# Optimization experiments

Hardware: AMD Instinct MI355X
Metric: run time of the kernel (lower is better)

The kernel has to match this reference:

```python
import jax, jax.numpy as jnp
import numpy as np

E, H = 1024, 16
HD = E // H
QLEN, KLEN, BS = 1024, 2048, 4
PREV = KLEN - QLEN


def _rel_shift(x):
    # x: (q, k, b, h) -> Transformer-XL relative shift
    q, k, b, h = x.shape
    x = jnp.pad(x, ((0, 0), (1, 0), (0, 0), (0, 0)))  # (q, k+1, b, h)
    x = x.reshape(k + 1, q, b, h)[1:].reshape(q, k, b, h)
    return x


def setup_inputs() -> dict:
    key = jax.random.key(0)
    ks = jax.random.split(key, 16)
    s = 0.02  # weight init scale
    inp = {
        "query": jax.random.normal(ks[0], (QLEN, BS, E), jnp.float32),
        "key": jax.random.normal(ks[1], (KLEN, BS, E), jnp.float32),
        "value": jax.random.normal(ks[2], (KLEN, BS, E), jnp.float32),
        "pos_embedding": jax.random.normal(ks[3], (KLEN, 1, E), jnp.float32),
        "U": jax.random.normal(ks[4], (H, HD), jnp.float32) * s,
        "V": jax.random.normal(ks[5], (H, HD), jnp.float32) * s,
        "Wq": jax.random.normal(ks[6], (E, E), jnp.float32) * s,
        "bq": jnp.zeros((E,), jnp.float32),
        "Wk": jax.random.normal(ks[7], (E, E), jnp.float32) * s,
        "bk": jnp.zeros((E,), jnp.float32),
        "Wv": jax.random.normal(ks[8], (E, E), jnp.float32) * s,
        "bv": jnp.zeros((E,), jnp.float32),
        "Wp": jax.random.normal(ks[9], (E, E), jnp.float32) * s,
        "Wo": jax.random.normal(ks[10], (E, E), jnp.float32) * s,
        "bo": jnp.zeros((E,), jnp.float32),
    }
    # causal XL mask: query i attends to keys j <= i + PREV; True = masked
    qi = jnp.arange(QLEN)[:, None]
    kj = jnp.arange(KLEN)[None, :]
    inp["mask"] = (kj > qi + PREV)[:, :, None]  # (q, k, 1) bool
    return inp


def reference(query, key, value, pos_embedding, U, V, Wq, bq, Wk, bk, Wv, bv, Wp, Wo, bo, mask):
    q_len, b, e = query.shape
    k_len = key.shape[0]
    scale = float(np.sqrt(e))  # note: sqrt(embed_dim), as in the source

    queries = (query @ Wq + bq).reshape(q_len, b, H, HD)
    keys = (key @ Wk + bk).reshape(k_len, b, H, HD)
    values = (value @ Wv + bv).reshape(k_len, b, H, HD)
    R = (pos_embedding @ Wp).reshape(-1, H, HD)  # (k, H, HD)

    content_score = jnp.einsum('qbhd,kbhd->qkbh', queries + U, keys)
    position_score = jnp.einsum('qbhd,khd->qkbh', queries + V, R)
    position_score = _rel_shift(position_score)

    attention_score = (content_score + position_score) / scale
    attention_score = jnp.where(mask[..., None], jnp.float32(-1e20), attention_score)
    attention = jax.nn.softmax(attention_score, axis=1)

    alpha = jnp.einsum('qkbh,kbhd->qbhd', attention, values).reshape(q_len, b, e)
    return alpha @ Wo + bo
```

## Files before the change

### kernel.cpp

```cpp
#include <hip/hip_runtime.h>
#include <stdint.h>

#define QLEN 1024
#define KLEN 2048
#define BSZ  4
#define NH   16
#define HD   64
#define EMB  1024
#define PREVL 1024
#define SLOG2E 0.045084220027780106f

typedef __attribute__((ext_vector_type(4))) float f32x4;
typedef __attribute__((ext_vector_type(8))) short bf16x8;
typedef __attribute__((ext_vector_type(4))) short bf16x4;

__device__ __forceinline__ unsigned short f2bf(float f){
  unsigned u = __float_as_uint(f);
  u += 0x7fffu + ((u >> 16) & 1u);
  return (unsigned short)(u >> 16);
}

__device__ __forceinline__ void gload_lds16(const void* g, void* l){
  __builtin_amdgcn_global_load_lds((const __attribute__((address_space(1))) void*)g,
                                   (__attribute__((address_space(3))) void*)l, 16, 0, 0);
}

__global__ void txl_transpose5(const float* __restrict__ w0, const float* __restrict__ w1,
                               const float* __restrict__ w2, const float* __restrict__ w3,
                               const float* __restrict__ w4,
                               unsigned short* __restrict__ o0, unsigned short* __restrict__ o1,
                               unsigned short* __restrict__ o2, unsigned short* __restrict__ o3,
                               unsigned short* __restrict__ o4){
  const float* in; unsigned short* out;
  switch (blockIdx.z){
    case 0: in = w0; out = o0; break;
    case 1: in = w1; out = o1; break;
    case 2: in = w2; out = o2; break;
    case 3: in = w3; out = o3; break;
    default: in = w4; out = o4; break;
  }
  __shared__ float tile[32][33];
  int tx = threadIdx.x, ty = threadIdx.y;
  int k0 = blockIdx.y * 32, n0 = blockIdx.x * 32;
  #pragma unroll
  for (int j = 0; j < 32; j += 8)
    tile[ty + j][tx] = in[(size_t)(k0 + ty + j) * EMB + n0 + tx];
  __syncthreads();
  #pragma unroll
  for (int j = 0; j < 32; j += 8)
    out[(size_t)(n0 + ty + j) * EMB + k0 + tx] = f2bf(tile[tx][ty + j]);
}

__global__ void txl_cvt(const float* __restrict__ q, const float* __restrict__ k,
                        const float* __restrict__ v, const float* __restrict__ p,
                        unsigned short* __restrict__ qo, unsigned short* __restrict__ ko,
                        unsigned short* __restrict__ vo, unsigned short* __restrict__ po){
  for (size_t c = (size_t)blockIdx.x * 256 + threadIdx.x; c < 2883584; c += (size_t)2048 * 256){
    const float* src; unsigned short* dst; size_t off;
    if (c < 524288)      { src = q; dst = qo; off = c; }
    else if (c < 1572864){ src = k; dst = ko; off = c - 524288; }
    else if (c < 2621440){ src = v; dst = vo; off = c - 1572864; }
    else                 { src = p; dst = po; off = c - 2621440; }
    f32x4 a = *(const f32x4*)(src + off * 8);
    f32x4 b = *(const f32x4*)(src + off * 8 + 4);
    bf16x8 r;
    #pragma unroll
    for (int u = 0; u < 4; ++u){ r[u] = (short)f2bf(a[u]); r[u + 4] = (short)f2bf(b[u]); }
    *(bf16x8*)(dst + off * 8) = r;
  }
}

template<int MODE>
__global__ __launch_bounds__(256)
void txl_gemm(const unsigned short* __restrict__ Ag, const unsigned short* __restrict__ Wt,
              const float* __restrict__ bias, const float* __restrict__ Ub,
              const float* __restrict__ Vb, void* __restrict__ out0,
              void* __restrict__ out1){
  const int tid = threadIdx.x;
  const int lane = tid & 63, wave = tid >> 6;
  const int lr = lane & 15, lg = lane >> 4;
  const int wm = wave >> 1, wn = wave & 1;
  const int m0 = blockIdx.y * 128, n0 = blockIdx.x * 128;
  __shared__ unsigned short At[128 * 64];
  __shared__ unsigned short Bt[128 * 64];
  f32x4 acc[4][4] = {};

  for (int kt = 0; kt < EMB / 64; ++kt){
    const int k0 = kt * 64;
    __syncthreads();
    #pragma unroll
    for (int j = 0; j < 4; ++j){
      int row = j * 32 + (tid >> 3);
      int g = (tid & 7) ^ (row & 7);
      gload_lds16(Ag + (size_t)(m0 + row) * EMB + k0 + g * 8, &At[j * 2048 + wave * 512]);
      gload_lds16(Wt + (size_t)(n0 + row) * EMB + k0 + g * 8, &Bt[j * 2048 + wave * 512]);
    }
    __syncthreads();
    #pragma unroll
    for (int ks = 0; ks < 2; ++ks){
      bf16x8 af[4], bfr[4];
      #pragma unroll
      for (int mb = 0; mb < 4; ++mb){
        int row = wm * 64 + mb * 16 + lr;
        af[mb] = *(const bf16x8*)&At[row * 64 + ((lg + 4 * ks) ^ (row & 7)) * 8];
      }
      #pragma unroll
      for (int nb = 0; nb < 4; ++nb){
        int row = wn * 64 + nb * 16 + lr;
        bfr[nb] = *(const bf16x8*)&Bt[row * 64 + ((lg + 4 * ks) ^ (row & 7)) * 8];
      }
      __builtin_amdgcn_s_setprio(1);
      #pragma unroll
      for (int mb = 0; mb < 4; ++mb)
        #pragma unroll
        for (int nb = 0; nb < 4; ++nb)
          acc[mb][nb] = __builtin_amdgcn_mfma_f32_16x16x32_bf16(af[mb], bfr[nb], acc[mb][nb], 0, 0, 0);
      __builtin_amdgcn_s_setprio(0);
    }
  }
  #pragma unroll
  for (int mb = 0; mb < 4; ++mb){
    #pragma unroll
    for (int nb = 0; nb < 4; ++nb){
      #pragma unroll
      for (int i = 0; i < 4; ++i){
        int m = m0 + wm * 64 + mb * 16 + 4 * lg + i;
        int n = n0 + wn * 64 + nb * 16 + lr;
        float v = acc[mb][nb][i];
        if constexpr (MODE == 0){
          int q = m >> 2, b = m & 3, h = n >> 6, d = n & 63;
          size_t idx = ((((size_t)b * NH + h) * QLEN) + q) * HD + d;
          float base = v + bias[n];
          ((unsigned short*)out0)[idx] = f2bf((base + Ub[n]) * SLOG2E);
          ((unsigned short*)out1)[idx] = f2bf((base + Vb[n]) * SLOG2E);
        } else if constexpr (MODE == 1){
          int kp = m >> 2, b = m & 3, h = n >> 6, d = n & 63;
          ((unsigned short*)out0)[((((size_t)b * NH + h) * KLEN) + kp) * HD + d] = f2bf(v + bias[n]);
        } else if constexpr (MODE == 2){
          int kp = m >> 2, b = m & 3, h = n >> 6, d = n & 63;
          ((unsigned short*)out0)[((((size_t)b * NH + h) * HD) + d) * KLEN + kp] = f2bf(v + bias[n]);
        } else if constexpr (MODE == 3){
          int h = n >> 6, d = n & 63;
          ((unsigned short*)out0)[((size_t)h * KLEN + m) * HD + d] = f2bf(v);
        } else {
          ((float*)out0)[(size_t)m * EMB + n] = v + bias[n];
        }
      }
    }
  }
}

__global__ __launch_bounds__(256)
void txl_attn(const unsigned short* __restrict__ Qu, const unsigned short* __restrict__ Qv,
              const unsigned short* __restrict__ Kb, const unsigned short* __restrict__ Vt,
              const unsigned short* __restrict__ Rb, unsigned short* __restrict__ alpha){
  const int tid = threadIdx.x, lane = tid & 63, wave = tid >> 6;
  const int lr = lane & 15, lg = lane >> 4;
  const int qt = blockIdx.x, h = blockIdx.y, b = blockIdx.z;
  const int q0 = qt * 64;
  const int myq0 = q0 + 16 * wave;

  __shared__ union { unsigned short q[2][64 * 64]; unsigned short p[4][16 * 64]; } smq;
  __shared__ unsigned short sm_k[64 * 64];
  __shared__ unsigned short sm_v[64 * 64];
  __shared__ unsigned short sm_r[128 * 64];
  __shared__ float sm_t[4][16 * 81];

  const unsigned short* quB = Qu + (((size_t)b * NH + h) * QLEN) * HD;
  const unsigned short* qvB = Qv + (((size_t)b * NH + h) * QLEN) * HD;
  const unsigned short* kB  = Kb + (((size_t)b * NH + h) * KLEN) * HD;
  const unsigned short* vB  = Vt + (((size_t)b * NH + h) * HD) * KLEN;
  const unsigned short* rB  = Rb + ((size_t)h * KLEN) * HD;

  #pragma unroll
  for (int j = 0; j < 2; ++j){
    int row = j * 32 + (tid >> 3);
    int g = (tid & 7) ^ (row & 7);
    gload_lds16(quB + (size_t)(q0 + row) * HD + g * 8, &smq.q[0][j * 2048 + wave * 512]);
    gload_lds16(qvB + (size_t)(q0 + row) * HD + g * 8, &smq.q[1][j * 2048 + wave * 512]);
  }
  __syncthreads();
  bf16x8 qfu[2], qfv[2];
  {
    int row = 16 * wave + lr;
    #pragma unroll
    for (int ks = 0; ks < 2; ++ks){
      qfu[ks] = *(const bf16x8*)&smq.q[0][row * 64 + ((lg + 4 * ks) ^ (row & 7)) * 8];
      qfv[ks] = *(const bf16x8*)&smq.q[1][row * 64 + ((lg + 4 * ks) ^ (row & 7)) * 8];
    }
  }

  f32x4 o[4] = {};
  float ls[4] = {0.f, 0.f, 0.f, 0.f};

  const int nk0 = qt + 17;
  const int nk = nk0 < 32 ? nk0 : 32;
  const int roff = 48 - 16 * wave;

  for (int kt = 0; kt < nk; ++kt){
    const int k0 = kt * 64;
    const int rbase = k0 + (QLEN - 64) - q0;
    __syncthreads();
    #pragma unroll
    for (int j = 0; j < 2; ++j){
      int row = j * 32 + (tid >> 3);
      int g = (tid & 7) ^ (row & 7);
      gload_lds16(kB + (size_t)(k0 + row) * HD + g * 8, &sm_k[j * 2048 + wave * 512]);
      gload_lds16(vB + (size_t)row * KLEN + k0 + g * 8, &sm_v[j * 2048 + wave * 512]);
    }
    #pragma unroll
    for (int j = 0; j < 4; ++j){
      int row = j * 32 + (tid >> 3);
      int g = (tid & 7) ^ (row & 7);
      int r = rbase + row; if (r > KLEN - 1) r = KLEN - 1;
      gload_lds16(rB + (size_t)r * HD + g * 8, &sm_r[j * 2048 + wave * 512]);
    }
    __syncthreads();

    f32x4 sc[4] = {};
    f32x4 tt[5] = {};
    __builtin_amdgcn_s_setprio(1);
    #pragma unroll
    for (int ks = 0; ks < 2; ++ks){
      #pragma unroll
      for (int nb = 0; nb < 4; ++nb){
        int row = nb * 16 + lr;
        bf16x8 kf = *(const bf16x8*)&sm_k[row * 64 + ((lg + 4 * ks) ^ (row & 7)) * 8];
        sc[nb] = __builtin_amdgcn_mfma_f32_16x16x32_bf16(qfu[ks], kf, sc[nb], 0, 0, 0);
      }
      #pragma unroll
      for (int rb = 0; rb < 5; ++rb){
        int row = roff + rb * 16 + lr;
        bf16x8 rf = *(const bf16x8*)&sm_r[row * 64 + ((lg + 4 * ks) ^ (row & 7)) * 8];
        tt[rb] = __builtin_amdgcn_mfma_f32_16x16x32_bf16(qfv[ks], rf, tt[rb], 0, 0, 0);
      }
    }
    __builtin_amdgcn_s_setprio(0);

    float* tw = sm_t[wave];
    #pragma unroll
    for (int rb = 0; rb < 5; ++rb)
      #pragma unroll
      for (int i = 0; i < 4; ++i)
        tw[(4 * lg + i) * 81 + rb * 16 + lr] = tt[rb][i];
    asm volatile("s_waitcnt lgkmcnt(0)" ::: "memory");

    #pragma unroll
    for (int i = 0; i < 4; ++i){
      int qq = 4 * lg + i;
      int qglob = myq0 + qq;
      float rs = 0.f;
      #pragma unroll
      for (int nb = 0; nb < 4; ++nb){
        int kk = nb * 16 + lr;
        float tv = tw[qq * 81 + kk + 15 - qq];
        float s = sc[nb][i] + tv;
        if (k0 + kk > qglob + PREVL) s = -1e30f;
        float p = exp2f(s);
        rs += p;
        smq.p[wave][qq * 64 + (((kk >> 3) ^ (qq & 7)) << 3) + (kk & 7)] = f2bf(p);
      }
      ls[i] += rs;
    }
    asm volatile("s_waitcnt lgkmcnt(0)" ::: "memory");

    __builtin_amdgcn_s_setprio(1);
    #pragma unroll
    for (int ks = 0; ks < 2; ++ks){
      bf16x8 pa = *(const bf16x8*)&smq.p[wave][lr * 64 + ((lg + 4 * ks) ^ (lr & 7)) * 8];
      #pragma unroll
      for (int db = 0; db < 4; ++db){
        int row = db * 16 + lr;
        bf16x8 vf = *(const bf16x8*)&sm_v[row * 64 + ((lg + 4 * ks) ^ (row & 7)) * 8];
        o[db] = __builtin_amdgcn_mfma_f32_16x16x32_bf16(pa, vf, o[db], 0, 0, 0);
      }
    }
    __builtin_amdgcn_s_setprio(0);
  }

  #pragma unroll
  for (int i = 0; i < 4; ++i){
    float s = ls[i];
    s += __shfl_xor(s, 1); s += __shfl_xor(s, 2);
    s += __shfl_xor(s, 4); s += __shfl_xor(s, 8);
    float inv = 1.0f / s;
    int q = myq0 + 4 * lg + i;
    #pragma unroll
    for (int db = 0; db < 4; ++db){
      int e = (h << 6) + db * 16 + lr;
      alpha[((size_t)q * BSZ + b) * EMB + e] = f2bf(o[db][i] * inv);
    }
  }
}

extern "C" void kernel_launch(void* const* d_in, const int* in_sizes, int n_in,
                              void* d_out, int out_size, void* d_ws, size_t ws_size,
                              hipStream_t stream) {
  const float* query = (const float*)d_in[0];
  const float* key   = (const float*)d_in[1];
  const float* value = (const float*)d_in[2];
  const float* pos   = (const float*)d_in[3];
  const float* U     = (const float*)d_in[4];
  const float* V     = (const float*)d_in[5];
  const float* Wq    = (const float*)d_in[6];
  const float* bq    = (const float*)d_in[7];
  const float* Wk    = (const float*)d_in[8];
  const float* bk    = (const float*)d_in[9];
  const float* Wv    = (const float*)d_in[10];
  const float* bv    = (const float*)d_in[11];
  const float* Wp    = (const float*)d_in[12];
  const float* Wo    = (const float*)d_in[13];
  const float* bo    = (const float*)d_in[14];

  char* w = (char*)d_ws;
  const size_t MB = 1u << 20;
  unsigned short* WqT = (unsigned short*)(w + 0 * MB);
  unsigned short* WkT = (unsigned short*)(w + 2 * MB);
  unsigned short* WvT = (unsigned short*)(w + 4 * MB);
  unsigned short* WpT = (unsigned short*)(w + 6 * MB);
  unsigned short* WoT = (unsigned short*)(w + 8 * MB);
  unsigned short* Qu  = (unsigned short*)(w + 10 * MB);
  unsigned short* Qv  = (unsigned short*)(w + 18 * MB);
  unsigned short* Kb  = (unsigned short*)(w + 26 * MB);
  unsigned short* Vt  = (unsigned short*)(w + 42 * MB);
  unsigned short* Rb  = (unsigned short*)(w + 58 * MB);
  unsigned short* qbf = (unsigned short*)(w + 62 * MB);
  unsigned short* kbf = (unsigned short*)(w + 70 * MB);
  unsigned short* vbf = (unsigned short*)(w + 86 * MB);
  unsigned short* pbf = (unsigned short*)(w + 102 * MB);
  unsigned short* alpha = qbf;

  txl_transpose5<<<dim3(32, 32, 5), dim3(32, 8), 0, stream>>>(Wq, Wk, Wv, Wp, Wo,
                                                              WqT, WkT, WvT, WpT, WoT);
  txl_cvt<<<dim3(2048), 256, 0, stream>>>(query, key, value, pos, qbf, kbf, vbf, pbf);

  txl_gemm<3><<<dim3(8, 16), 256, 0, stream>>>(pbf, WpT, nullptr, nullptr, nullptr, (void*)Rb, nullptr);
  txl_gemm<0><<<dim3(8, 32), 256, 0, stream>>>(qbf, WqT, bq, U, V, (void*)Qu, (void*)Qv);
  txl_gemm<1><<<dim3(8, 64), 256, 0, stream>>>(kbf, WkT, bk, nullptr, nullptr, (void*)Kb, nullptr);
  txl_gemm<2><<<dim3(8, 64), 256, 0, stream>>>(vbf, WvT, bv, nullptr, nullptr, (void*)Vt, nullptr);

  txl_attn<<<dim3(16, 16, 4), 256, 0, stream>>>(Qu, Qv, Kb, Vt, Rb, alpha);

  txl_gemm<4><<<dim3(8, 32), 256, 0, stream>>>(alpha, WoT, bo, nullptr, nullptr, d_out, nullptr);
}
```

Before: 295.7 us.

## Shrink attention LDS footprint with bf16 position tile and direct Q loads

Stores the per-wave position-score staging tile as bf16 instead of fp32, with a new odd padding, and gives the probability tile its own padded buffer. Q fragments are now loaded straight from global memory into registers instead of being staged through LDS with a block barrier. The aim is to cut LDS usage so more blocks fit per CU, and to remove the startup barrier. The cost is extra rounding of position scores to bf16 before the exponent, which loses accuracy. The 16-bit stores at odd padding may also cause bank conflicts or unaligned access.

```diff
diff --git a/kernel.cpp b/kernel.cpp
--- a/kernel.cpp
+++ b/kernel.cpp
@@ -14,10 +14,16 @@
 typedef __attribute__((ext_vector_type(8))) short bf16x8;
 typedef __attribute__((ext_vector_type(4))) short bf16x4;
 
+#define TPAD 83
+#define PPAD 72
+
 __device__ __forceinline__ unsigned short f2bf(float f){
   unsigned u = __float_as_uint(f);
   u += 0x7fffu + ((u >> 16) & 1u);
   return (unsigned short)(u >> 16);
+}
+__device__ __forceinline__ float bf2f(unsigned short s){
+  return __uint_as_float(((unsigned)s) << 16);
 }
 
 __device__ __forceinline__ void gload_lds16(const void* g, void* l){
@@ -160,11 +166,11 @@
   const int q0 = qt * 64;
   const int myq0 = q0 + 16 * wave;
 
-  __shared__ union { unsigned short q[2][64 * 64]; unsigned short p[4][16 * 64]; } smq;
+  __shared__ unsigned short sm_p[4][16 * PPAD];
   __shared__ unsigned short sm_k[64 * 64];
   __shared__ unsigned short sm_v[64 * 64];
   __shared__ unsigned short sm_r[128 * 64];
-  __shared__ float sm_t[4][16 * 81];
+  __shared__ unsigned short sm_t[4][16 * TPAD];
 
   const unsigned short* quB = Qu + (((size_t)b * NH + h) * QLEN) * HD;
   const unsigned short* qvB = Qv + (((size_t)b * NH + h) * QLEN) * HD;
@@ -172,21 +178,13 @@
   const unsigned short* vB  = Vt + (((size_t)b * NH + h) * HD) * KLEN;
   const unsigned short* rB  = Rb + ((size_t)h * KLEN) * HD;
 
-  #pragma unroll
-  for (int j = 0; j < 2; ++j){
-    int row = j * 32 + (tid >> 3);
-    int g = (tid & 7) ^ (row & 7);
-    gload_lds16(quB + (size_t)(q0 + row) * HD + g * 8, &smq.q[0][j * 2048 + wave * 512]);
-    gload_lds16(qvB + (size_t)(q0 + row) * HD + g * 8, &smq.q[1][j * 2048 + wave * 512]);
-  }
-  __syncthreads();
   bf16x8 qfu[2], qfv[2];
   {
-    int row = 16 * wave + lr;
+    int qrow = myq0 + lr;
     #pragma unroll
     for (int ks = 0; ks < 2; ++ks){
-      qfu[ks] = *(const bf16x8*)&smq.q[0][row * 64 + ((lg + 4 * ks) ^ (row & 7)) * 8];
-      qfv[ks] = *(const bf16x8*)&smq.q[1][row * 64 + ((lg + 4 * ks) ^ (row & 7)) * 8];
+      qfu[ks] = *(const bf16x8*)(quB + (size_t)qrow * HD + (lg + 4 * ks) * 8);
+      qfv[ks] = *(const bf16x8*)(qvB + (size_t)qrow * HD + (lg + 4 * ks) * 8);
     }
   }
 
@@ -237,12 +235,12 @@
     }
     __builtin_amdgcn_s_setprio(0);
 
-    float* tw = sm_t[wave];
+    unsigned short* tw = sm_t[wave];
     #pragma unroll
     for (int rb = 0; rb < 5; ++rb)
       #pragma unroll
       for (int i = 0; i < 4; ++i)
-        tw[(4 * lg + i) * 81 + rb * 16 + lr] = tt[rb][i];
+        tw[(4 * lg + i) * TPAD + rb * 16 + lr] = f2bf(tt[rb][i]);
     asm volatile("s_waitcnt lgkmcnt(0)" ::: "memory");
 
     #pragma unroll
@@ -253,12 +251,12 @@
       #pragma unroll
       for (int nb = 0; nb < 4; ++nb){
         int kk = nb * 16 + lr;
-        float tv = tw[qq * 81 + kk + 15 - qq];
+        float tv = bf2f(tw[qq * TPAD + kk + 15 - qq]);
         float s = sc[nb][i] + tv;
         if (k0 + kk > qglob + PREVL) s = -1e30f;
         float p = exp2f(s);
         rs += p;
-        smq.p[wave][qq * 64 + (((kk >> 3) ^ (qq & 7)) << 3) + (kk & 7)] = f2bf(p);
+        sm_p[wave][qq * PPAD + (((kk >> 3) ^ (qq & 7)) << 3) + (kk & 7)] = f2bf(p);
       }
       ls[i] += rs;
     }
@@ -267,7 +265,7 @@
     __builtin_amdgcn_s_setprio(1);
     #pragma unroll
     for (int ks = 0; ks < 2; ++ks){
-      bf16x8 pa = *(const bf16x8*)&smq.p[wave][lr * 64 + ((lg + 4 * ks) ^ (lr & 7)) * 8];
+      bf16x8 pa = *(const bf16x8*)&sm_p[wave][lr * PPAD + ((lg + 4 * ks) ^ (lr & 7)) * 8];
       #pragma unroll
       for (int db = 0; db < 4; ++db){
         int row = db * 16 + lr;
```

Measured after the change: 306.3 us. 3.6% more time.
